# Kernel optimization log

Measured on AMD Instinct MI355X. Metric: run time of the kernel, lower is better.

Reference implementation:

```python
import jax, jax.numpy as jnp
import numpy as np

DIM = 1024

def setup_inputs() -> dict:
    key = jax.random.key(0)
    k1, k2, k3, k4, k5 = jax.random.split(key, 5)
    B, S, D = 32, 2048, DIM
    hidden_state = jax.random.normal(k1, (B, D), dtype=jnp.float32)
    encoder_outputs = jax.random.normal(k2, (B, S, D), dtype=jnp.float32)
    # linear1: (2D -> D) with bias; linear2: (D -> 1) no bias
    W1 = jax.random.normal(k3, (2 * D, D), dtype=jnp.float32) / np.sqrt(2 * D)
    b1 = jnp.zeros((D,), dtype=jnp.float32)
    w2 = jax.random.normal(k4, (D,), dtype=jnp.float32) / np.sqrt(D)
    return {"hidden_state": hidden_state, "encoder_outputs": encoder_outputs,
            "W1": W1, "b1": b1, "w2": w2}

def reference(hidden_state, encoder_outputs, W1, b1, w2):
    B, S, D = encoder_outputs.shape
    # concat(encoder_outputs, broadcast hidden) @ W1 == enc @ W1_enc + hid @ W1_hid
    W1_enc, W1_hid = W1[:D], W1[D:]                      # each [D, D]
    enc_proj = jnp.einsum('bsd,de->bse', encoder_outputs, W1_enc)
    hid_proj = jnp.einsum('bd,de->be', hidden_state, W1_hid)
    h = jnp.tanh(enc_proj + hid_proj[:, None, :] + b1)    # [B, S, D]
    e = jnp.einsum('bsd,d->bs', h, w2)                    # [B, S]
    alpha = jax.nn.softmax(e, axis=1)                     # [B, S]
    context = jnp.einsum('bs,bsd->bd', alpha, encoder_outputs)  # [B, D]
    return context
```

## Files before the change

kernel.cpp:

```cpp
#include <hip/hip_runtime.h>
#include <hip/hip_bf16.h>
#include <cstdint>

typedef __bf16 bf16;
typedef __bf16 bf16x8 __attribute__((ext_vector_type(8)));
typedef float  f32x4  __attribute__((ext_vector_type(4)));

#define P_W1BT   0u
#define P_C      2097152u
#define P_E      2228224u
#define P_ALPHA  2490368u
#define P_TOTAL  2752512ull

#define O_W1BT   0u
#define O_C      2097152u
#define O_E      2228224u
#define O_ALPHA  2490368u
#define O_HIDP   2752512u
#define O_CTXP   3801088u
#define O_TOTAL  5898240ull

__global__ __launch_bounds__(256) void k_pre(const float* __restrict__ W1,
                                             const float* __restrict__ b1,
                                             bf16* __restrict__ w1bt,
                                             float* __restrict__ cvec,
                                             float* __restrict__ ebuf,
                                             float* __restrict__ out) {
    int bid = blockIdx.x, t = threadIdx.x;
    if (bid < 1024) {
        __shared__ float tile[32][33];
        int bx = bid & 31, by = bid >> 5;
        int tx = t & 31, ty = t >> 5;
#pragma unroll
        for (int i = 0; i < 4; ++i)
            tile[ty + i * 8][tx] = W1[(size_t)(by * 32 + ty + i * 8) * 1024 + bx * 32 + tx];
        __syncthreads();
#pragma unroll
        for (int i = 0; i < 4; ++i)
            w1bt[(size_t)(bx * 32 + ty + i * 8) * 1024 + by * 32 + tx] = (bf16)tile[tx][ty + i * 8];
    } else if (bid < 1408) {
        int idx = (bid - 1024) * 256 + t;
        if (idx < 32768) cvec[idx] = b1[idx & 1023];
        else             ebuf[idx - 32768] = 0.f;
    } else {
        out[(bid - 1408) * 256 + t] = 0.f;
    }
}

__global__ void k_hid_atomic(const float* __restrict__ hid, const float* __restrict__ W1,
                             float* __restrict__ cvec) {
    int e = blockIdx.x * 256 + threadIdx.x;
    int dch = blockIdx.y;
    float acc[32];
#pragma unroll
    for (int b = 0; b < 32; ++b) acc[b] = 0.f;
    int d0 = dch * 32;
#pragma unroll 4
    for (int dd = 0; dd < 32; ++dd) {
        int d = d0 + dd;
        float w = W1[(size_t)(1024 + d) * 1024 + e];
#pragma unroll
        for (int b = 0; b < 32; ++b) acc[b] += hid[b * 1024 + d] * w;
    }
#pragma unroll
    for (int b = 0; b < 32; ++b) atomicAdd(&cvec[b * 1024 + e], acc[b]);
}

__device__ inline float fast_tanh(float x) {
    float e2 = __expf(2.f * x);
    return 1.f - 2.f / (e2 + 1.f);
}

#define SBAR  __builtin_amdgcn_s_barrier()
#define VMC6  asm volatile("s_waitcnt vmcnt(6)" ::: "memory")
#define VMC0  asm volatile("s_waitcnt vmcnt(0)" ::: "memory")
#define PRIO1 __builtin_amdgcn_s_setprio(1)
#define PRIO0 __builtin_amdgcn_s_setprio(0)

__global__ __launch_bounds__(512, 1) void k_gemm9(
    const float* __restrict__ encf, const bf16* __restrict__ w1bt,
    const float* __restrict__ cvec, const float* __restrict__ w2,
    float* __restrict__ ebuf)
{
    __shared__ __align__(16) char smem[147456];
    const int t = threadIdx.x;
    const int lane = t & 63;
    const int w  = t >> 6;
    const int wr = w >> 2;
    const int wc = w & 3;
    const int l15 = lane & 15, g = (lane >> 4) & 3;

    unsigned raw = blockIdx.x;
    unsigned swz = (raw & 7u) * 128u + (raw >> 3);
    const int nt = swz & 3, mt = swz >> 2;
    const int m0 = mt * 256, n0 = nt * 256;
    const int b  = m0 >> 11;

    const int r6  = t >> 3;
    const int gsA = (t & 7) ^ (r6 & 7);
    const char* srcA = (const char*)encf + (size_t)(m0 + r6) * 4096 + gsA * 16;
    const int r2  = t >> 2;
    const int gsB = (t & 3) ^ ((r2 >> 1) & 3);
    const char* srcB = (const char*)w1bt + (size_t)(n0 + r2) * 2048 + gsB * 16;

#define STAGE_A(D, T) do { \
    _Pragma("unroll") \
    for (int h = 0; h < 4; ++h) \
        __builtin_amdgcn_global_load_lds( \
            (const __attribute__((address_space(1))) unsigned int*)(srcA + (size_t)h * 262144 + (size_t)(T) * 128), \
            (__attribute__((address_space(3))) unsigned int*)(smem + (D) * 49152 + h * 8192 + t * 16), 16, 0, 0); \
} while (0)
#define STAGE_B(D, T) do { \
    _Pragma("unroll") \
    for (int h = 0; h < 2; ++h) \
        __builtin_amdgcn_global_load_lds( \
            (const __attribute__((address_space(1))) unsigned int*)(srcB + (size_t)h * 262144 + (size_t)(T) * 64), \
            (__attribute__((address_space(3))) unsigned int*)(smem + (D) * 49152 + 32768 + h * 8192 + t * 16), 16, 0, 0); \
} while (0)

    const int rbA = wr * 128 + l15;
    const int rbB = wc * 64 + l15;
    const int sAlo = ((2 * g) ^ (l15 & 7)) << 4;
    const int sAhi = ((2 * g + 1) ^ (l15 & 7)) << 4;
    const int sB   = (g ^ ((l15 >> 1) & 3)) << 4;

    f32x4 acc[8][4] = {};
    bf16x8 fa[8], fb[4];

    float wv[4];
    int gcol[4];
#pragma unroll
    for (int n = 0; n < 4; ++n) {
        gcol[n] = n0 + wc * 64 + n * 16 + l15;
        wv[n] = w2[gcol[n]];
    }

#define RDFRAGS(D) do { \
    _Pragma("unroll") \
    for (int m = 0; m < 8; ++m) { \
        const char* _p = smem + (D) * 49152 + (rbA + m * 16) * 128; \
        f32x4 lo = *(const f32x4*)(_p + sAlo); \
        f32x4 hi = *(const f32x4*)(_p + sAhi); \
        bf16x8 a; \
        a[0]=(bf16)lo[0]; a[1]=(bf16)lo[1]; a[2]=(bf16)lo[2]; a[3]=(bf16)lo[3]; \
        a[4]=(bf16)hi[0]; a[5]=(bf16)hi[1]; a[6]=(bf16)hi[2]; a[7]=(bf16)hi[3]; \
        fa[m] = a; \
    } \
    _Pragma("unroll") \
    for (int n = 0; n < 4; ++n) \
        fb[n] = *(const bf16x8*)(smem + (D) * 49152 + 32768 + (rbB + n * 16) * 64 + sB); \
} while (0)

#define MFMA32() do { \
    PRIO1; \
    _Pragma("unroll") \
    for (int m = 0; m < 8; ++m) \
        _Pragma("unroll") \
        for (int n = 0; n < 4; ++n) \
            acc[m][n] = __builtin_amdgcn_mfma_f32_16x16x32_bf16(fa[m], fb[n], acc[m][n], 0, 0, 0); \
    PRIO0; \
} while (0)

    STAGE_A(0, 0); STAGE_B(0, 0);
    STAGE_A(1, 1); STAGE_B(1, 1);
    VMC6; SBAR;

#pragma unroll 1
    for (int tt = 0; tt < 30; tt += 3) {
        RDFRAGS(0);
        STAGE_A(2, tt + 2); STAGE_B(2, tt + 2);
        MFMA32();
        VMC6; SBAR;

        RDFRAGS(1);
        STAGE_A(0, tt + 3); STAGE_B(0, tt + 3);
        MFMA32();
        VMC6; SBAR;

        RDFRAGS(2);
        STAGE_A(1, tt + 4); STAGE_B(1, tt + 4);
        MFMA32();
        VMC6; SBAR;
    }
    RDFRAGS(0);
    MFMA32();
    VMC0; SBAR;
    RDFRAGS(1);
    MFMA32();

    float cv[4];
#pragma unroll
    for (int n = 0; n < 4; ++n) cv[n] = cvec[b * 1024 + gcol[n]];
#pragma unroll
    for (int m = 0; m < 8; ++m) {
#pragma unroll
        for (int r = 0; r < 4; ++r) {
            float s = 0.f;
#pragma unroll
            for (int n = 0; n < 4; ++n)
                s += fast_tanh(acc[m][n][r] + cv[n]) * wv[n];
            s += __shfl_xor(s, 1); s += __shfl_xor(s, 2);
            s += __shfl_xor(s, 4); s += __shfl_xor(s, 8);
            if (l15 == 0)
                atomicAdd(&ebuf[m0 + wr * 128 + m * 16 + g * 4 + r], s);
        }
    }
#undef STAGE_A
#undef STAGE_B
#undef RDFRAGS
#undef MFMA32
}

__global__ void k_softmax(const float* __restrict__ ebuf, float* __restrict__ alpha) {
    int bb = blockIdx.x, t = threadIdx.x;
    __shared__ float red[4], red2[4];
    float v[8];
    float mx = -1e30f;
#pragma unroll
    for (int i = 0; i < 8; ++i) { v[i] = ebuf[bb * 2048 + i * 256 + t]; mx = fmaxf(mx, v[i]); }
    for (int o = 32; o > 0; o >>= 1) mx = fmaxf(mx, __shfl_xor(mx, o));
    if ((t & 63) == 0) red[t >> 6] = mx;
    __syncthreads();
    mx = fmaxf(fmaxf(red[0], red[1]), fmaxf(red[2], red[3]));
    float sum = 0.f;
#pragma unroll
    for (int i = 0; i < 8; ++i) { v[i] = __expf(v[i] - mx); sum += v[i]; }
    for (int o = 32; o > 0; o >>= 1) sum += __shfl_xor(sum, o);
    if ((t & 63) == 0) red2[t >> 6] = sum;
    __syncthreads();
    sum = red2[0] + red2[1] + red2[2] + red2[3];
    float inv = 1.f / sum;
#pragma unroll
    for (int i = 0; i < 8; ++i) alpha[bb * 2048 + i * 256 + t] = v[i] * inv;
}

__global__ void k_ctx_f(const float* __restrict__ enc, const float* __restrict__ alpha,
                        float* __restrict__ out) {
    int bid = blockIdx.x;
    int bb = bid >> 4, sc = bid & 15;
    int t = threadIdx.x;
    __shared__ float al[128];
    if (t < 128) al[t] = alpha[bb * 2048 + sc * 128 + t];
    __syncthreads();
    f32x4 acc = {0.f, 0.f, 0.f, 0.f};
    const f32x4* base = (const f32x4*)(enc + ((size_t)bb * 2048 + sc * 128) * 1024) + t;
    for (int s = 0; s < 128; ++s) {
        f32x4 vv = base[(size_t)s * 256];
        acc += vv * al[s];
    }
    float* o = out + (size_t)bb * 1024 + t * 4;
    atomicAdd(&o[0], acc[0]);
    atomicAdd(&o[1], acc[1]);
    atomicAdd(&o[2], acc[2]);
    atomicAdd(&o[3], acc[3]);
}

__global__ void k_hid_partial(const float* __restrict__ hid, const float* __restrict__ W1,
                              float* __restrict__ hidp) {
    int e = blockIdx.x * 256 + threadIdx.x;
    int dch = blockIdx.y;
    float acc[32];
#pragma unroll
    for (int b = 0; b < 32; ++b) acc[b] = 0.f;
    int d0 = dch * 128;
    for (int dd = 0; dd < 128; ++dd) {
        int d = d0 + dd;
        float w = W1[(size_t)(1024 + d) * 1024 + e];
#pragma unroll
        for (int b = 0; b < 32; ++b) acc[b] += hid[b * 1024 + d] * w;
    }
#pragma unroll
    for (int b = 0; b < 32; ++b) hidp[((size_t)dch * 32 + b) * 1024 + e] = acc[b];
}

__global__ void k_hid_reduce(const float* __restrict__ hidp, const float* __restrict__ b1,
                             float* __restrict__ cvec) {
    int i = blockIdx.x * 256 + threadIdx.x;
    int e = i & 1023;
    float s = b1[e];
#pragma unroll
    for (int dch = 0; dch < 8; ++dch) s += hidp[(size_t)dch * 32768 + i];
    cvec[i] = s;
}

__global__ void k_w1t(const float* __restrict__ W1, bf16* __restrict__ w1bt) {
    __shared__ float tile[32][33];
    int tx = threadIdx.x, ty = threadIdx.y;
    int bx = blockIdx.x, by = blockIdx.y;
#pragma unroll
    for (int i = 0; i < 4; ++i)
        tile[ty + i * 8][tx] = W1[(size_t)(by * 32 + ty + i * 8) * 1024 + bx * 32 + tx];
    __syncthreads();
#pragma unroll
    for (int i = 0; i < 4; ++i)
        w1bt[(size_t)(bx * 32 + ty + i * 8) * 1024 + by * 32 + tx] = (bf16)tile[tx][ty + i * 8];
}

__global__ __launch_bounds__(256, 3) void k_gemm_e(
    const float* __restrict__ enc, const bf16* __restrict__ w1bt,
    const float* __restrict__ cvec, const float* __restrict__ w2,
    float* __restrict__ ebuf)
{
    __shared__ __align__(16) unsigned char smem[24 * 1024];
    const int t = threadIdx.x;
    const int lane = t & 63;
    const int w = t >> 6;
    const int wr = w >> 1, wc = w & 1;
    const int l15 = lane & 15, g = lane >> 4;

    unsigned raw = blockIdx.x;
    unsigned swz = (raw & 7u) * 512u + (raw >> 3);
    const int nt = swz & 7, mt = swz >> 3;
    const int m0 = mt * 128, n0 = nt * 128;
    const int b = m0 >> 11;

    int rowA = (t >> 3);
    int slotA = (t & 7) ^ (rowA & 7);
    const char* gA0 = (const char*)enc + (size_t)(m0 + rowA) * 4096 + slotA * 16;
    int rowB = (t >> 2);
    int slotB = (t & 3) ^ ((t >> 3) & 3);
    const char* gB0 = (const char*)w1bt + (size_t)(n0 + rowB) * 2048 + slotB * 16;

    int rowA0 = wr * 64 + l15;
    unsigned offA0 = (unsigned)rowA0 * 128 + ((((2 * g)) ^ (l15 & 7)) << 4);
    int rowB0 = wc * 64 + l15;
    unsigned offB0 = 16384u + (unsigned)rowB0 * 64 + (((g ^ ((l15 >> 1) & 3))) << 4);

    f32x4 acc[4][4] = {};

    for (int kt = 0; kt < 32; ++kt) {
        const char* pa = gA0 + kt * 128;
        const char* pb = gB0 + kt * 64;
#pragma unroll
        for (int c = 0; c < 4; ++c)
            __builtin_amdgcn_global_load_lds(
                (const __attribute__((address_space(1))) unsigned int*)(pa + (size_t)c * 131072),
                (__attribute__((address_space(3))) unsigned int*)(smem + c * 4096 + w * 1024), 16, 0, 0);
#pragma unroll
        for (int c = 0; c < 2; ++c)
            __builtin_amdgcn_global_load_lds(
                (const __attribute__((address_space(1))) unsigned int*)(pb + (size_t)c * 131072),
                (__attribute__((address_space(3))) unsigned int*)(smem + 16384 + c * 4096 + w * 1024), 16, 0, 0);
        __syncthreads();

        bf16x8 af[4], bfr[4];
#pragma unroll
        for (int m = 0; m < 4; ++m) {
            unsigned o0 = offA0 + m * 2048;
            f32x4 lo = *(const f32x4*)(smem + o0);
            f32x4 hi = *(const f32x4*)(smem + (o0 ^ 16u));
            bf16x8 a;
            a[0] = (bf16)lo[0]; a[1] = (bf16)lo[1]; a[2] = (bf16)lo[2]; a[3] = (bf16)lo[3];
            a[4] = (bf16)hi[0]; a[5] = (bf16)hi[1]; a[6] = (bf16)hi[2]; a[7] = (bf16)hi[3];
            af[m] = a;
        }
#pragma unroll
        for (int n = 0; n < 4; ++n)
            bfr[n] = *(const bf16x8*)(smem + (offB0 + n * 1024));
#pragma unroll
        for (int m = 0; m < 4; ++m)
#pragma unroll
            for (int n = 0; n < 4; ++n)
                acc[m][n] = __builtin_amdgcn_mfma_f32_16x16x32_bf16(af[m], bfr[n], acc[m][n], 0, 0, 0);
        __syncthreads();
    }

    float cv[4], wv[4];
#pragma unroll
    for (int n = 0; n < 4; ++n) {
        int gcol = n0 + wc * 64 + n * 16 + l15;
        cv[n] = cvec[b * 1024 + gcol];
        wv[n] = w2[gcol];
    }
#pragma unroll
    for (int m = 0; m < 4; ++m) {
#pragma unroll
        for (int r = 0; r < 4; ++r) {
            float s = 0.f;
#pragma unroll
            for (int n = 0; n < 4; ++n)
                s += fast_tanh(acc[m][n][r] + cv[n]) * wv[n];
            s += __shfl_xor(s, 1); s += __shfl_xor(s, 2);
            s += __shfl_xor(s, 4); s += __shfl_xor(s, 8);
            if (l15 == 0)
                atomicAdd(&ebuf[m0 + wr * 64 + m * 16 + g * 4 + r], s);
        }
    }
}

__global__ void k_ctx_partial(const float* __restrict__ enc, const float* __restrict__ alpha,
                              float* __restrict__ ctxp) {
    int bid = blockIdx.x;
    int bb = bid >> 4, sc = bid & 15;
    int t = threadIdx.x;
    __shared__ float al[128];
    if (t < 128) al[t] = alpha[bb * 2048 + sc * 128 + t];
    __syncthreads();
    f32x4 acc = {0.f, 0.f, 0.f, 0.f};
    const f32x4* base = (const f32x4*)(enc + ((size_t)bb * 2048 + sc * 128) * 1024) + t;
    for (int s = 0; s < 128; ++s) {
        f32x4 vv = base[(size_t)s * 256];
        acc += vv * al[s];
    }
    *((f32x4*)(ctxp + (size_t)bid * 1024) + t) = acc;
}

__global__ void k_ctx_reduce(const float* __restrict__ ctxp, float* __restrict__ out) {
    int i = blockIdx.x * 256 + threadIdx.x;
    int bb = i >> 10, d = i & 1023;
    float s = 0.f;
#pragma unroll
    for (int sc = 0; sc < 16; ++sc) s += ctxp[((size_t)(bb * 16 + sc)) * 1024 + d];
    out[i] = s;
}

extern "C" void kernel_launch(void* const* d_in, const int* in_sizes, int n_in,
                              void* d_out, int out_size, void* d_ws, size_t ws_size,
                              hipStream_t stream) {
    const float* hid = (const float*)d_in[0];
    const float* enc = (const float*)d_in[1];
    const float* W1  = (const float*)d_in[2];
    const float* b1  = (const float*)d_in[3];
    const float* w2  = (const float*)d_in[4];
    float* out = (float*)d_out;
    char* ws = (char*)d_ws;

    if (ws_size >= O_TOTAL) {
        bf16*  w1bt  = (bf16*)(ws + P_W1BT);
        float* cvec  = (float*)(ws + P_C);
        float* ebuf  = (float*)(ws + P_E);
        float* alpha = (float*)(ws + P_ALPHA);

        k_pre<<<1536, 256, 0, stream>>>(W1, b1, w1bt, cvec, ebuf, out);
        k_hid_atomic<<<dim3(4, 32), 256, 0, stream>>>(hid, W1, cvec);
        k_gemm9<<<1024, 512, 0, stream>>>(enc, w1bt, cvec, w2, ebuf);
        k_softmax<<<32, 256, 0, stream>>>(ebuf, alpha);
        k_ctx_f<<<512, 256, 0, stream>>>(enc, alpha, out);
    } else {
        bf16*  w1bt  = (bf16*)(ws + O_W1BT);
        float* cvec  = (float*)(ws + O_C);
        float* ebuf  = (float*)(ws + O_E);
        float* alpha = (float*)(ws + O_ALPHA);
        float* hidp  = (float*)(ws + O_HIDP);
        float* ctxp  = (float*)(ws + O_CTXP);

        hipMemsetAsync(ebuf, 0, 65536 * sizeof(float), stream);
        k_hid_partial<<<dim3(4, 8), 256, 0, stream>>>(hid, W1, hidp);
        k_w1t<<<dim3(32, 32), dim3(32, 8), 0, stream>>>(W1, w1bt);
        k_hid_reduce<<<128, 256, 0, stream>>>(hidp, b1, cvec);
        k_gemm_e<<<4096, 256, 0, stream>>>(enc, w1bt, cvec, w2, ebuf);
        k_softmax<<<32, 256, 0, stream>>>(ebuf, alpha);
        k_ctx_partial<<<512, 256, 0, stream>>>(enc, alpha, ctxp);
        k_ctx_reduce<<<128, 256, 0, stream>>>(ctxp, out);
    }
}
```

Measured before the change: 262.4 us.

## Halve GEMM M-tile and use double buffering to raise occupancy

The fused encoder GEMM drops its M-tile from 256 to 128 rows and replaces the triple-buffered LDS pipeline with double buffering. LDS use falls from 144KB to 64KB, and launch bounds now request several blocks per CU, so more waves can run concurrently to hide latency. In exchange, each block does half the MFMA work per B tile, which doubles reads of the W1 tiles. Each stage also waits for all outstanding loads (vmcnt 0), so prefetch depth is shallower.

```diff
diff --git a/kernel.cpp b/kernel.cpp
--- a/kernel.cpp
+++ b/kernel.cpp
@@ -72,17 +72,16 @@
 }
 
 #define SBAR  __builtin_amdgcn_s_barrier()
-#define VMC6  asm volatile("s_waitcnt vmcnt(6)" ::: "memory")
 #define VMC0  asm volatile("s_waitcnt vmcnt(0)" ::: "memory")
 #define PRIO1 __builtin_amdgcn_s_setprio(1)
 #define PRIO0 __builtin_amdgcn_s_setprio(0)
 
-__global__ __launch_bounds__(512, 1) void k_gemm9(
+__global__ __launch_bounds__(512, 4) void k_gemm10(
     const float* __restrict__ encf, const bf16* __restrict__ w1bt,
     const float* __restrict__ cvec, const float* __restrict__ w2,
     float* __restrict__ ebuf)
 {
-    __shared__ __align__(16) char smem[147456];
+    __shared__ __align__(16) char smem[65536];
     const int t = threadIdx.x;
     const int lane = t & 63;
     const int w  = t >> 6;
@@ -91,9 +90,9 @@
     const int l15 = lane & 15, g = (lane >> 4) & 3;
 
     unsigned raw = blockIdx.x;
-    unsigned swz = (raw & 7u) * 128u + (raw >> 3);
+    unsigned swz = (raw & 7u) * 256u + (raw >> 3);
     const int nt = swz & 3, mt = swz >> 2;
-    const int m0 = mt * 256, n0 = nt * 256;
+    const int m0 = mt * 128, n0 = nt * 256;
     const int b  = m0 >> 11;
 
     const int r6  = t >> 3;
@@ -105,27 +104,27 @@
 
 #define STAGE_A(D, T) do { \
     _Pragma("unroll") \
-    for (int h = 0; h < 4; ++h) \
+    for (int h = 0; h < 2; ++h) \
         __builtin_amdgcn_global_load_lds( \
             (const __attribute__((address_space(1))) unsigned int*)(srcA + (size_t)h * 262144 + (size_t)(T) * 128), \
-            (__attribute__((address_space(3))) unsigned int*)(smem + (D) * 49152 + h * 8192 + t * 16), 16, 0, 0); \
+            (__attribute__((address_space(3))) unsigned int*)(smem + (D) * 32768 + h * 8192 + t * 16), 16, 0, 0); \
 } while (0)
 #define STAGE_B(D, T) do { \
     _Pragma("unroll") \
     for (int h = 0; h < 2; ++h) \
         __builtin_amdgcn_global_load_lds( \
             (const __attribute__((address_space(1))) unsigned int*)(srcB + (size_t)h * 262144 + (size_t)(T) * 64), \
-            (__attribute__((address_space(3))) unsigned int*)(smem + (D) * 49152 + 32768 + h * 8192 + t * 16), 16, 0, 0); \
+            (__attribute__((address_space(3))) unsigned int*)(smem + (D) * 32768 + 16384 + h * 8192 + t * 16), 16, 0, 0); \
 } while (0)
 
-    const int rbA = wr * 128 + l15;
+    const int rbA = wr * 64 + l15;
     const int rbB = wc * 64 + l15;
     const int sAlo = ((2 * g) ^ (l15 & 7)) << 4;
-    const int sAhi = ((2 * g + 1) ^ (l15 & 7)) << 4;
+    const int sAhi = sAlo ^ 16;
     const int sB   = (g ^ ((l15 >> 1) & 3)) << 4;
 
-    f32x4 acc[8][4] = {};
-    bf16x8 fa[8], fb[4];
+    f32x4 acc[4][4] = {};
+    bf16x8 fa[4], fb[4];
 
     float wv[4];
     int gcol[4];
@@ -137,8 +136,8 @@
 
 #define RDFRAGS(D) do { \
     _Pragma("unroll") \
-    for (int m = 0; m < 8; ++m) { \
-        const char* _p = smem + (D) * 49152 + (rbA + m * 16) * 128; \
+    for (int m = 0; m < 4; ++m) { \
+        const char* _p = smem + (D) * 32768 + (rbA + m * 16) * 128; \
         f32x4 lo = *(const f32x4*)(_p + sAlo); \
         f32x4 hi = *(const f32x4*)(_p + sAhi); \
         bf16x8 a; \
@@ -148,13 +147,13 @@
     } \
     _Pragma("unroll") \
     for (int n = 0; n < 4; ++n) \
-        fb[n] = *(const bf16x8*)(smem + (D) * 49152 + 32768 + (rbB + n * 16) * 64 + sB); \
+        fb[n] = *(const bf16x8*)(smem + (D) * 32768 + 16384 + (rbB + n * 16) * 64 + sB); \
 } while (0)
 
-#define MFMA32() do { \
+#define MFMA16() do { \
     PRIO1; \
     _Pragma("unroll") \
-    for (int m = 0; m < 8; ++m) \
+    for (int m = 0; m < 4; ++m) \
         _Pragma("unroll") \
         for (int n = 0; n < 4; ++n) \
             acc[m][n] = __builtin_amdgcn_mfma_f32_16x16x32_bf16(fa[m], fb[n], acc[m][n], 0, 0, 0); \
@@ -162,37 +161,26 @@
 } while (0)
 
     STAGE_A(0, 0); STAGE_B(0, 0);
-    STAGE_A(1, 1); STAGE_B(1, 1);
-    VMC6; SBAR;
+    VMC0; SBAR;
 
 #pragma unroll 1
-    for (int tt = 0; tt < 30; tt += 3) {
+    for (int tt = 0; tt < 32; tt += 2) {
+        STAGE_A(1, tt + 1); STAGE_B(1, tt + 1);
         RDFRAGS(0);
-        STAGE_A(2, tt + 2); STAGE_B(2, tt + 2);
-        MFMA32();
-        VMC6; SBAR;
-
+        MFMA16();
+        VMC0; SBAR;
+
+        if (tt + 2 < 32) { STAGE_A(0, tt + 2); STAGE_B(0, tt + 2); }
         RDFRAGS(1);
-        STAGE_A(0, tt + 3); STAGE_B(0, tt + 3);
-        MFMA32();
-        VMC6; SBAR;
-
-        RDFRAGS(2);
-        STAGE_A(1, tt + 4); STAGE_B(1, tt + 4);
-        MFMA32();
-        VMC6; SBAR;
-    }
-    RDFRAGS(0);
-    MFMA32();
-    VMC0; SBAR;
-    RDFRAGS(1);
-    MFMA32();
+        MFMA16();
+        VMC0; SBAR;
+    }
 
     float cv[4];
 #pragma unroll
     for (int n = 0; n < 4; ++n) cv[n] = cvec[b * 1024 + gcol[n]];
 #pragma unroll
-    for (int m = 0; m < 8; ++m) {
+    for (int m = 0; m < 4; ++m) {
 #pragma unroll
         for (int r = 0; r < 4; ++r) {
             float s = 0.f;
@@ -202,13 +190,13 @@
             s += __shfl_xor(s, 1); s += __shfl_xor(s, 2);
             s += __shfl_xor(s, 4); s += __shfl_xor(s, 8);
             if (l15 == 0)
-                atomicAdd(&ebuf[m0 + wr * 128 + m * 16 + g * 4 + r], s);
+                atomicAdd(&ebuf[m0 + wr * 64 + m * 16 + g * 4 + r], s);
         }
     }
 #undef STAGE_A
 #undef STAGE_B
 #undef RDFRAGS
-#undef MFMA32
+#undef MFMA16
 }
 
 __global__ void k_softmax(const float* __restrict__ ebuf, float* __restrict__ alpha) {
@@ -433,7 +421,7 @@
 
         k_pre<<<1536, 256, 0, stream>>>(W1, b1, w1bt, cvec, ebuf, out);
         k_hid_atomic<<<dim3(4, 32), 256, 0, stream>>>(hid, W1, cvec);
-        k_gemm9<<<1024, 512, 0, stream>>>(enc, w1bt, cvec, w2, ebuf);
+        k_gemm10<<<2048, 512, 0, stream>>>(enc, w1bt, cvec, w2, ebuf);
         k_softmax<<<32, 256, 0, stream>>>(ebuf, alpha);
         k_ctx_f<<<512, 256, 0, stream>>>(enc, alpha, out);
     } else {
```

Result: slower. 281.3 us (+7.2%).

## Stage fp32 A tile through registers as bf16 with double-buffered LDS

Applied to the files above, without the earlier changes.

The GEMM kernel used to DMA fp32 encoder tiles straight into LDS through a triple buffer and convert them to bf16 at every fragment read. Now each thread loads the fp32 A data into registers, converts it to bf16 once, and writes it into a smaller swizzled double-buffered LDS region. This halves A-tile LDS space and removes the repeated conversion work in the inner loop. In exchange the pipeline is shallower, and the register-staged global loads add register pressure and waitcnt coupling.

```diff
diff --git a/kernel.cpp b/kernel.cpp
--- a/kernel.cpp
+++ b/kernel.cpp
@@ -72,17 +72,18 @@
 }
 
 #define SBAR  __builtin_amdgcn_s_barrier()
-#define VMC6  asm volatile("s_waitcnt vmcnt(6)" ::: "memory")
+#define VMC4  asm volatile("s_waitcnt vmcnt(4)" ::: "memory")
 #define VMC0  asm volatile("s_waitcnt vmcnt(0)" ::: "memory")
+#define LGKM0 asm volatile("s_waitcnt lgkmcnt(0)" ::: "memory")
 #define PRIO1 __builtin_amdgcn_s_setprio(1)
 #define PRIO0 __builtin_amdgcn_s_setprio(0)
 
-__global__ __launch_bounds__(512, 1) void k_gemm9(
+__global__ __launch_bounds__(512, 1) void k_gemm11(
     const float* __restrict__ encf, const bf16* __restrict__ w1bt,
     const float* __restrict__ cvec, const float* __restrict__ w2,
     float* __restrict__ ebuf)
 {
-    __shared__ __align__(16) char smem[147456];
+    __shared__ __align__(16) char smem[65536];
     const int t = threadIdx.x;
     const int lane = t & 63;
     const int w  = t >> 6;
@@ -96,33 +97,47 @@
     const int m0 = mt * 256, n0 = nt * 256;
     const int b  = m0 >> 11;
 
-    const int r6  = t >> 3;
-    const int gsA = (t & 7) ^ (r6 & 7);
-    const char* srcA = (const char*)encf + (size_t)(m0 + r6) * 4096 + gsA * 16;
+    const int arow  = t >> 1;
+    const int ahalf = t & 1;
+    const int akey  = (arow >> 1) & 3;
+    const int ap0   = ((ahalf * 2)     ^ akey) << 4;
+    const int ap1   = ((ahalf * 2 + 1) ^ akey) << 4;
+    const float* aSrc = encf + (size_t)(m0 + arow) * 1024 + ahalf * 16;
+    const unsigned aDst = (unsigned)arow * 64;
+
     const int r2  = t >> 2;
     const int gsB = (t & 3) ^ ((r2 >> 1) & 3);
     const char* srcB = (const char*)w1bt + (size_t)(n0 + r2) * 2048 + gsB * 16;
 
-#define STAGE_A(D, T) do { \
-    _Pragma("unroll") \
-    for (int h = 0; h < 4; ++h) \
-        __builtin_amdgcn_global_load_lds( \
-            (const __attribute__((address_space(1))) unsigned int*)(srcA + (size_t)h * 262144 + (size_t)(T) * 128), \
-            (__attribute__((address_space(3))) unsigned int*)(smem + (D) * 49152 + h * 8192 + t * 16), 16, 0, 0); \
+    f32x4 ra0, ra1, ra2, ra3;
+
+#define ISSUE_A(T) do { \
+    const float* _s = aSrc + (size_t)(T) * 32; \
+    ra0 = *(const f32x4*)(_s);      ra1 = *(const f32x4*)(_s + 4); \
+    ra2 = *(const f32x4*)(_s + 8);  ra3 = *(const f32x4*)(_s + 12); \
 } while (0)
-#define STAGE_B(D, T) do { \
+
+#define WRITE_A(OFF) do { \
+    bf16x8 _p0, _p1; \
+    _p0[0]=(bf16)ra0[0]; _p0[1]=(bf16)ra0[1]; _p0[2]=(bf16)ra0[2]; _p0[3]=(bf16)ra0[3]; \
+    _p0[4]=(bf16)ra1[0]; _p0[5]=(bf16)ra1[1]; _p0[6]=(bf16)ra1[2]; _p0[7]=(bf16)ra1[3]; \
+    _p1[0]=(bf16)ra2[0]; _p1[1]=(bf16)ra2[1]; _p1[2]=(bf16)ra2[2]; _p1[3]=(bf16)ra2[3]; \
+    _p1[4]=(bf16)ra3[0]; _p1[5]=(bf16)ra3[1]; _p1[6]=(bf16)ra3[2]; _p1[7]=(bf16)ra3[3]; \
+    *(bf16x8*)(smem + (OFF) + aDst + ap0) = _p0; \
+    *(bf16x8*)(smem + (OFF) + aDst + ap1) = _p1; \
+} while (0)
+
+#define STAGE_B(OFF, T) do { \
     _Pragma("unroll") \
     for (int h = 0; h < 2; ++h) \
         __builtin_amdgcn_global_load_lds( \
             (const __attribute__((address_space(1))) unsigned int*)(srcB + (size_t)h * 262144 + (size_t)(T) * 64), \
-            (__attribute__((address_space(3))) unsigned int*)(smem + (D) * 49152 + 32768 + h * 8192 + t * 16), 16, 0, 0); \
+            (__attribute__((address_space(3))) unsigned int*)(smem + (OFF) + 16384 + h * 8192 + t * 16), 16, 0, 0); \
 } while (0)
 
     const int rbA = wr * 128 + l15;
     const int rbB = wc * 64 + l15;
-    const int sAlo = ((2 * g) ^ (l15 & 7)) << 4;
-    const int sAhi = ((2 * g + 1) ^ (l15 & 7)) << 4;
-    const int sB   = (g ^ ((l15 >> 1) & 3)) << 4;
+    const int sAB = (g ^ ((l15 >> 1) & 3)) << 4;
 
     f32x4 acc[8][4] = {};
     bf16x8 fa[8], fb[4];
@@ -135,20 +150,13 @@
         wv[n] = w2[gcol[n]];
     }
 
-#define RDFRAGS(D) do { \
+#define RDFRAGS(OFF) do { \
     _Pragma("unroll") \
-    for (int m = 0; m < 8; ++m) { \
-        const char* _p = smem + (D) * 49152 + (rbA + m * 16) * 128; \
-        f32x4 lo = *(const f32x4*)(_p + sAlo); \
-        f32x4 hi = *(const f32x4*)(_p + sAhi); \
-        bf16x8 a; \
-        a[0]=(bf16)lo[0]; a[1]=(bf16)lo[1]; a[2]=(bf16)lo[2]; a[3]=(bf16)lo[3]; \
-        a[4]=(bf16)hi[0]; a[5]=(bf16)hi[1]; a[6]=(bf16)hi[2]; a[7]=(bf16)hi[3]; \
-        fa[m] = a; \
-    } \
+    for (int m = 0; m < 8; ++m) \
+        fa[m] = *(const bf16x8*)(smem + (OFF) + (rbA + m * 16) * 64 + sAB); \
     _Pragma("unroll") \
     for (int n = 0; n < 4; ++n) \
-        fb[n] = *(const bf16x8*)(smem + (D) * 49152 + 32768 + (rbB + n * 16) * 64 + sB); \
+        fb[n] = *(const bf16x8*)(smem + (OFF) + 16384 + (rbB + n * 16) * 64 + sAB); \
 } while (0)
 
 #define MFMA32() do { \
@@ -161,32 +169,31 @@
     PRIO0; \
 } while (0)
 
-    STAGE_A(0, 0); STAGE_B(0, 0);
-    STAGE_A(1, 1); STAGE_B(1, 1);
-    VMC6; SBAR;
-
+    ISSUE_A(0);
+    STAGE_B(0, 0);
+    WRITE_A(0);
+    ISSUE_A(1);
+    VMC4;
+    LGKM0; SBAR;
+
+    int dOff = 0;
 #pragma unroll 1
-    for (int tt = 0; tt < 30; tt += 3) {
-        RDFRAGS(0);
-        STAGE_A(2, tt + 2); STAGE_B(2, tt + 2);
+    for (int tt = 0; tt < 32; ++tt) {
+        const int nOff = dOff ^ 32768;
+        if (tt < 31) {
+            STAGE_B(nOff, tt + 1);
+            WRITE_A(nOff);
+        }
+        if (tt < 30) ISSUE_A(tt + 2);
+        RDFRAGS(dOff);
         MFMA32();
-        VMC6; SBAR;
-
-        RDFRAGS(1);
-        STAGE_A(0, tt + 3); STAGE_B(0, tt + 3);
-        MFMA32();
-        VMC6; SBAR;
-
-        RDFRAGS(2);
-        STAGE_A(1, tt + 4); STAGE_B(1, tt + 4);
-        MFMA32();
-        VMC6; SBAR;
-    }
-    RDFRAGS(0);
-    MFMA32();
-    VMC0; SBAR;
-    RDFRAGS(1);
-    MFMA32();
+        if (tt < 31) {
+            if (tt < 30) { VMC4; }
+            else         { VMC0; }
+            LGKM0; SBAR;
+            dOff = nOff;
+        }
+    }
 
     float cv[4];
 #pragma unroll
@@ -205,7 +212,8 @@
                 atomicAdd(&ebuf[m0 + wr * 128 + m * 16 + g * 4 + r], s);
         }
     }
-#undef STAGE_A
+#undef ISSUE_A
+#undef WRITE_A
 #undef STAGE_B
 #undef RDFRAGS
 #undef MFMA32
@@ -433,7 +441,7 @@
 
         k_pre<<<1536, 256, 0, stream>>>(W1, b1, w1bt, cvec, ebuf, out);
         k_hid_atomic<<<dim3(4, 32), 256, 0, stream>>>(hid, W1, cvec);
-        k_gemm9<<<1024, 512, 0, stream>>>(enc, w1bt, cvec, w2, ebuf);
+        k_gemm11<<<1024, 512, 0, stream>>>(enc, w1bt, cvec, w2, ebuf);
         k_softmax<<<32, 256, 0, stream>>>(ebuf, alpha);
         k_ctx_f<<<512, 256, 0, stream>>>(enc, alpha, out);
     } else {
```

Result: slower. 270.4 us (+3.0%).
